# Optimization experiments

Hardware: AMD Instinct MI355X
Metric: run time of the kernel (lower is better)

The kernel has to match this reference:

```python
import jax, jax.numpy as jnp
import numpy as np
from jax import lax

NUM_GRID = 64
NUM_PATCHES = NUM_GRID * NUM_GRID  # 4096
BATCH = 4
ITERATION = 10


def setup_inputs() -> dict:
    key = jax.random.key(0)
    k1, k2, k3 = jax.random.split(key, 3)
    delta_p = jax.random.normal(k1, (BATCH, NUM_GRID, NUM_GRID, 2), dtype=jnp.float32)
    logits = jax.random.normal(k2, (BATCH, NUM_PATCHES, 1), dtype=jnp.float32)
    # learned pairwise weight; original inits to zeros, use small randn for nontrivial signal
    W = jax.random.normal(k3, (1, NUM_PATCHES, NUM_PATCHES), dtype=jnp.float32) * 0.01
    return {"delta_p": delta_p, "logits": logits, "W": W}


def reference(delta_p, logits, W):
    b, g, _, _ = delta_p.shape
    n = g * g
    feats = delta_p.reshape(b, n, 2)                              # (b, N, 2)
    feats_norm = jnp.linalg.norm(feats, axis=2, keepdims=True)    # (b, N, 1)
    pairwise_norm = feats_norm * jnp.swapaxes(feats_norm, 1, 2)   # (b, N, N) outer product
    pairwise_dot = jnp.einsum('bnd,bmd->bnm', feats, feats)       # (b, N, N)
    pairwise_sim = pairwise_dot / pairwise_norm
    sq = feats_norm ** 2                                          # (b, N, 1)
    gaussian = jnp.exp(-(sq + jnp.swapaxes(sq, 1, 2)) / 2)        # broadcast instead of tile
    W_sym = (W + jnp.swapaxes(W, 1, 2)) / 2                       # (1, N, N)
    pairwise_potential = gaussian * (1 - pairwise_sim) * W_sym    # (b, N, N)

    unary = logits

    def body(i, l):
        # probs*PP - (1-probs)*PP summed over j == PP @ (2*sigmoid(l) - 1)
        m = 2.0 * jax.nn.sigmoid(l[..., 0]) - 1.0                 # (b, N)
        E = jnp.einsum('bnm,bm->bn', pairwise_potential, m)[..., None]
        return unary + E

    logits = lax.fori_loop(0, ITERATION, body, logits)
    return logits
```

## Files before the change

kernel.cpp:

```cpp
#include <hip/hip_runtime.h>
#include <math.h>

#define NN 4096
#define NB 4
#define NITER 10
#define ROWS 16
#define TW 512

typedef _Float16 f16x8 __attribute__((ext_vector_type(8)));
typedef float f32x4 __attribute__((ext_vector_type(4)));

__device__ __align__(16) float gA [NB * NN];
__device__ __align__(16) float gUx[NB * NN];
__device__ __align__(16) float gUy[NB * NN];
__device__ __align__(16) unsigned short gTh[2][12 * NN];

__device__ inline unsigned short f16b(float x) {
    _Float16 h = (_Float16)x;
    return *(unsigned short*)&h;
}
__device__ inline unsigned f16pair(float x, float y) {
    return (unsigned)f16b(x) | ((unsigned)f16b(y) << 16);
}

__global__ __launch_bounds__(256) void stats_kernel(const float* __restrict__ dp,
                                                    const float* __restrict__ logits) {
    int i = blockIdx.x * 256 + threadIdx.x;
    int b = i >> 12, n = i & 4095;
    float x = dp[2 * i], y = dp[2 * i + 1];
    float sq = x * x + y * y;
    float av = expf(-0.5f * sq);
    float inv = 1.0f / sqrtf(sq);
    float uxv = x * inv, uyv = y * inv;
    gA[i] = av; gUx[i] = uxv; gUy[i] = uyv;
    float l = logits[i];
    float mv = 2.0f / (1.0f + expf(-l)) - 1.0f;
    float t0 = av * mv;
    gTh[0][(3 * b + 0) * NN + n] = f16b(t0);
    gTh[0][(3 * b + 1) * NN + n] = f16b(t0 * uxv);
    gTh[0][(3 * b + 2) * NN + n] = f16b(t0 * uyv);
}

__global__ __launch_bounds__(256) void wsym_kernel(const float* __restrict__ W,
                                                   unsigned* __restrict__ Sb) {
    __shared__ float At[64][65];
    __shared__ float Bt[64][65];
    int idx = blockIdx.x, bi = 0, rem = 64;
    while (idx >= rem) { idx -= rem; ++bi; --rem; }
    int bj = bi + idx;
    int r0 = threadIdx.x >> 4;
    int c4 = (threadIdx.x & 15) * 4;
#pragma unroll
    for (int i = 0; i < 4; ++i) {
        int r = r0 + i * 16;
        float4 va = *(const float4*)&W[(size_t)(bi * 64 + r) * NN + bj * 64 + c4];
        float4 vb = *(const float4*)&W[(size_t)(bj * 64 + r) * NN + bi * 64 + c4];
        At[r][c4 + 0] = va.x; At[r][c4 + 1] = va.y;
        At[r][c4 + 2] = va.z; At[r][c4 + 3] = va.w;
        Bt[r][c4 + 0] = vb.x; Bt[r][c4 + 1] = vb.y;
        Bt[r][c4 + 2] = vb.z; Bt[r][c4 + 3] = vb.w;
    }
    __syncthreads();
    int tp = threadIdx.x & 31;
    int rr = threadIdx.x >> 5;
#pragma unroll
    for (int i = 0; i < 8; ++i) {
        int r = rr + i * 8;
        int c0 = 2 * tp, c1 = c0 + 1;
        float v0 = 0.5f * (At[r][c0] + Bt[c0][r]);
        float v1 = 0.5f * (At[r][c1] + Bt[c1][r]);
        Sb[(size_t)(bi * 64 + r) * 2048 + bj * 32 + tp] = f16pair(v0, v1);
        float u0 = 0.5f * (Bt[r][c0] + At[c0][r]);
        float u1 = 0.5f * (Bt[r][c1] + At[c1][r]);
        Sb[(size_t)(bj * 64 + r) * 2048 + bi * 32 + tp] = f16pair(u0, u1);
    }
}

__global__ __launch_bounds__(TW) void matvec_kernel(const unsigned short* __restrict__ Wh,
    const float* __restrict__ logits, float* __restrict__ out, int rd, int last) {
    __shared__ __align__(16) unsigned short Tl[12 * NN];
    __shared__ __align__(16) float Ered[8][64][4];
    __shared__ float El[16][17];

    const int tid = threadIdx.x;

#pragma unroll
    for (int c = 0; c < 12; ++c) {
        int koct = tid;
        uint4 v = *(const uint4*)(gTh[rd] + c * NN + koct * 8);
        int gs = (c * 512 + koct) ^ (c & 7);
        *(uint4*)(Tl + gs * 8) = v;
    }
    __syncthreads();

    const int w = tid >> 6, lane = tid & 63;
    const int mrow = lane & 15, grp = lane >> 4;
    const int row0 = blockIdx.x * ROWS;
    const int kbase = w * 512;
    const unsigned short* Wp = Wh + (size_t)(row0 + mrow) * NN + kbase + grp * 8;

    const int cc = mrow;
    const bool cok = (cc < 12);
    const int gbase = cc * 512 + (kbase >> 3) + grp;

    f32x4 acc = {0.f, 0.f, 0.f, 0.f};
#pragma unroll
    for (int mf = 0; mf < 16; ++mf) {
        f16x8 a = *(const f16x8*)(Wp + mf * 32);
        f16x8 b = {};
        if (cok) {
            int gs = (gbase + mf * 4) ^ (cc & 7);
            b = *(const f16x8*)(Tl + gs * 8);
        }
        acc = __builtin_amdgcn_mfma_f32_16x16x32_f16(a, b, acc, 0, 0, 0);
    }
    *(f32x4*)Ered[w][lane] = acc;
    __syncthreads();

    if (tid < 64) {
        f32x4 s = {};
#pragma unroll
        for (int ww = 0; ww < 8; ++ww) s += *(const f32x4*)Ered[ww][tid];
        int rr = tid >> 4, c = tid & 15;
#pragma unroll
        for (int r = 0; r < 4; ++r) El[rr * 4 + r][c] = s[r];
    }
    __syncthreads();

    if (tid < 64) {
        int b = tid >> 4, r = tid & 15;
        int m = row0 + r, idx = b * NN + m;
        float S0 = El[r][3 * b], S1 = El[r][3 * b + 1], S2 = El[r][3 * b + 2];
        float av = gA[idx], uxv = gUx[idx], uyv = gUy[idx];
        float l = logits[idx] + av * (S0 - uxv * S1 - uyv * S2);
        if (last) {
            out[idx] = l;
        } else {
            float mv = 2.0f / (1.0f + expf(-l)) - 1.0f;
            float t0 = av * mv;
            unsigned short* Td = gTh[rd ^ 1];
            Td[(3 * b + 0) * NN + m] = f16b(t0);
            Td[(3 * b + 1) * NN + m] = f16b(t0 * uxv);
            Td[(3 * b + 2) * NN + m] = f16b(t0 * uyv);
        }
    }
}

extern "C" void kernel_launch(void* const* d_in, const int* in_sizes, int n_in,
                              void* d_out, int out_size, void* d_ws, size_t ws_size,
                              hipStream_t stream) {
    const float* delta_p = (const float*)d_in[0];
    const float* logits  = (const float*)d_in[1];
    const float* W       = (const float*)d_in[2];
    float* out = (float*)d_out;

    unsigned* Wb = (unsigned*)d_ws;
    const unsigned short* Wh = (const unsigned short*)d_ws;

    stats_kernel<<<64, 256, 0, stream>>>(delta_p, logits);
    wsym_kernel<<<2080, 256, 0, stream>>>(W, Wb);

    for (int it = 0; it < NITER; ++it)
        matvec_kernel<<<256, TW, 0, stream>>>(Wh, logits, out, it & 1,
                                              it == NITER - 1 ? 1 : 0);
}
```

Before: 101.8 us.

## Merge setup kernels and prefetch W into registers before per-warp T staging

```diff
diff --git a/kernel.cpp b/kernel.cpp
--- a/kernel.cpp
+++ b/kernel.cpp
@@ -6,6 +6,7 @@
 #define NITER 10
 #define ROWS 16
 #define TW 512
+#define WSYM_BLOCKS 2080
 
 typedef _Float16 f16x8 __attribute__((ext_vector_type(8)));
 typedef float f32x4 __attribute__((ext_vector_type(4)));
@@ -23,26 +24,26 @@
     return (unsigned)f16b(x) | ((unsigned)f16b(y) << 16);
 }
 
-__global__ __launch_bounds__(256) void stats_kernel(const float* __restrict__ dp,
-                                                    const float* __restrict__ logits) {
-    int i = blockIdx.x * 256 + threadIdx.x;
-    int b = i >> 12, n = i & 4095;
-    float x = dp[2 * i], y = dp[2 * i + 1];
-    float sq = x * x + y * y;
-    float av = expf(-0.5f * sq);
-    float inv = 1.0f / sqrtf(sq);
-    float uxv = x * inv, uyv = y * inv;
-    gA[i] = av; gUx[i] = uxv; gUy[i] = uyv;
-    float l = logits[i];
-    float mv = 2.0f / (1.0f + expf(-l)) - 1.0f;
-    float t0 = av * mv;
-    gTh[0][(3 * b + 0) * NN + n] = f16b(t0);
-    gTh[0][(3 * b + 1) * NN + n] = f16b(t0 * uxv);
-    gTh[0][(3 * b + 2) * NN + n] = f16b(t0 * uyv);
-}
-
-__global__ __launch_bounds__(256) void wsym_kernel(const float* __restrict__ W,
-                                                   unsigned* __restrict__ Sb) {
+__global__ __launch_bounds__(256) void head_kernel(const float* __restrict__ W,
+    unsigned* __restrict__ Sb, const float* __restrict__ dp,
+    const float* __restrict__ logits) {
+    if (blockIdx.x >= WSYM_BLOCKS) {
+        int i = (blockIdx.x - WSYM_BLOCKS) * 256 + threadIdx.x;
+        int b = i >> 12, n = i & 4095;
+        float x = dp[2 * i], y = dp[2 * i + 1];
+        float sq = x * x + y * y;
+        float av = expf(-0.5f * sq);
+        float inv = 1.0f / sqrtf(sq);
+        float uxv = x * inv, uyv = y * inv;
+        gA[i] = av; gUx[i] = uxv; gUy[i] = uyv;
+        float l = logits[i];
+        float mv = 2.0f / (1.0f + expf(-l)) - 1.0f;
+        float t0 = av * mv;
+        gTh[0][(3 * b + 0) * NN + n] = f16b(t0);
+        gTh[0][(3 * b + 1) * NN + n] = f16b(t0 * uxv);
+        gTh[0][(3 * b + 2) * NN + n] = f16b(t0 * uyv);
+        return;
+    }
     __shared__ float At[64][65];
     __shared__ float Bt[64][65];
     int idx = blockIdx.x, bi = 0, rem = 64;
@@ -76,43 +77,43 @@
     }
 }
 
-__global__ __launch_bounds__(TW) void matvec_kernel(const unsigned short* __restrict__ Wh,
+__global__ void __launch_bounds__(TW) matvec_kernel(const unsigned short* __restrict__ Wh,
     const float* __restrict__ logits, float* __restrict__ out, int rd, int last) {
-    __shared__ __align__(16) unsigned short Tl[12 * NN];
+    __shared__ __align__(16) unsigned short Tl[8][12 * 512];
     __shared__ __align__(16) float Ered[8][64][4];
     __shared__ float El[16][17];
 
     const int tid = threadIdx.x;
-
-#pragma unroll
-    for (int c = 0; c < 12; ++c) {
-        int koct = tid;
-        uint4 v = *(const uint4*)(gTh[rd] + c * NN + koct * 8);
-        int gs = (c * 512 + koct) ^ (c & 7);
-        *(uint4*)(Tl + gs * 8) = v;
-    }
-    __syncthreads();
-
     const int w = tid >> 6, lane = tid & 63;
     const int mrow = lane & 15, grp = lane >> 4;
     const int row0 = blockIdx.x * ROWS;
     const int kbase = w * 512;
     const unsigned short* Wp = Wh + (size_t)(row0 + mrow) * NN + kbase + grp * 8;
-
     const int cc = mrow;
     const bool cok = (cc < 12);
-    const int gbase = cc * 512 + (kbase >> 3) + grp;
+    const unsigned short* Tcur = gTh[rd];
+
+    f16x8 areg[16];
+#pragma unroll
+    for (int mf = 0; mf < 16; ++mf) areg[mf] = *(const f16x8*)(Wp + mf * 32);
+
+    unsigned short* Tw = &Tl[w][0];
+#pragma unroll
+    for (int c = 0; c < 12; ++c) {
+        uint4 v = *(const uint4*)(Tcur + c * NN + kbase + lane * 8);
+        int g = (c * 64 + lane) ^ (c & 7);
+        *(uint4*)(Tw + g * 8) = v;
+    }
 
     f32x4 acc = {0.f, 0.f, 0.f, 0.f};
 #pragma unroll
     for (int mf = 0; mf < 16; ++mf) {
-        f16x8 a = *(const f16x8*)(Wp + mf * 32);
         f16x8 b = {};
         if (cok) {
-            int gs = (gbase + mf * 4) ^ (cc & 7);
-            b = *(const f16x8*)(Tl + gs * 8);
+            int g = (cc * 64 + mf * 4 + grp) ^ (cc & 7);
+            b = *(const f16x8*)(Tw + g * 8);
         }
-        acc = __builtin_amdgcn_mfma_f32_16x16x32_f16(a, b, acc, 0, 0, 0);
+        acc = __builtin_amdgcn_mfma_f32_16x16x32_f16(areg[mf], b, acc, 0, 0, 0);
     }
     *(f32x4*)Ered[w][lane] = acc;
     __syncthreads();
@@ -157,8 +158,7 @@
     unsigned* Wb = (unsigned*)d_ws;
     const unsigned short* Wh = (const unsigned short*)d_ws;
 
-    stats_kernel<<<64, 256, 0, stream>>>(delta_p, logits);
-    wsym_kernel<<<2080, 256, 0, stream>>>(W, Wb);
+    head_kernel<<<WSYM_BLOCKS + 64, 256, 0, stream>>>(W, Wb, delta_p, logits);
 
     for (int it = 0; it < NITER; ++it)
         matvec_kernel<<<256, TW, 0, stream>>>(Wh, logits, out, it & 1,
```

New measurement: 96.73 us (median of 2 runs). 1.05x faster.
